# Optimization experiments

Hardware: AMD Instinct MI355X
Metric: run time of the kernel (lower is better)

Reference implementation:

```python
import jax, jax.numpy as jnp
import numpy as np

B, S, HID = 2, 2048, 2048
NH, NKV, HD = 16, 4, 128
ROT = 64            # head_dim * partial_rotary_factor
WINDOW = 512        # sliding_window_size
ROPE_BASE = 10000.0


def setup_inputs() -> dict:
    key = jax.random.key(0)
    ks = jax.random.split(key, 5)
    scale = 0.02
    return {
        "hidden_states": jax.random.normal(ks[0], (B, S, HID), jnp.float32),
        "Wq": jax.random.normal(ks[1], (NH * HD, HID), jnp.float32) * scale,
        "Wk": jax.random.normal(ks[2], (NKV * HD, HID), jnp.float32) * scale,
        "Wv": jax.random.normal(ks[3], (NKV * HD, HID), jnp.float32) * scale,
        "Wo": jax.random.normal(ks[4], (HID, NH * HD), jnp.float32) * scale,
    }


def _rope_cos_sin(seq_len, dtype):
    inv_freq = 1.0 / (ROPE_BASE ** (jnp.arange(0, ROT, 2, dtype=jnp.float32) / ROT))
    t = jnp.arange(seq_len, dtype=jnp.float32)
    freqs = t[:, None] * inv_freq[None, :]          # [S, ROT/2]
    emb = jnp.concatenate([freqs, freqs], axis=-1)   # [S, ROT]
    return jnp.cos(emb).astype(dtype), jnp.sin(emb).astype(dtype)


def _rotate_half(x):
    x1, x2 = x[..., : x.shape[-1] // 2], x[..., x.shape[-1] // 2:]
    return jnp.concatenate([-x2, x1], axis=-1)


def reference(hidden_states, Wq, Wk, Wv, Wo):
    b, s, _ = hidden_states.shape
    n_rep = NH // NKV

    q = (hidden_states @ Wq.T).reshape(b, s, NH, HD).transpose(0, 2, 1, 3)    # [B,NH,S,HD]
    k = (hidden_states @ Wk.T).reshape(b, s, NKV, HD).transpose(0, 2, 1, 3)   # [B,NKV,S,HD]
    v = (hidden_states @ Wv.T).reshape(b, s, NKV, HD).transpose(0, 2, 1, 3)

    # partial rotary embedding on the first ROT dims
    cos, sin = _rope_cos_sin(s, q.dtype)   # [S, ROT]
    cos = cos[None, None]                  # broadcast over batch, heads
    sin = sin[None, None]
    q_rot, q_pass = q[..., :ROT], q[..., ROT:]
    k_rot, k_pass = k[..., :ROT], k[..., ROT:]
    q_rot = q_rot * cos + _rotate_half(q_rot) * sin
    k_rot = k_rot * cos + _rotate_half(k_rot) * sin
    q = jnp.concatenate([q_rot, q_pass], axis=-1)
    k = jnp.concatenate([k_rot, k_pass], axis=-1)

    # GQA: repeat kv heads
    k = jnp.repeat(k, n_rep, axis=1)   # [B,NH,S,HD]
    v = jnp.repeat(v, n_rep, axis=1)

    scores = jnp.einsum("bhqd,bhkd->bhqk", q, k) / jnp.sqrt(jnp.asarray(HD, q.dtype))

    # sliding-window causal mask: allow j in [i-WINDOW+1, i]
    i = jnp.arange(s)[:, None]
    j = jnp.arange(s)[None, :]
    allowed = (j <= i) & (j > i - WINDOW)
    scores = jnp.where(allowed[None, None], scores, -jnp.inf)

    attn = jax.nn.softmax(scores.astype(jnp.float32), axis=-1).astype(q.dtype)
    out = jnp.einsum("bhqk,bhkd->bhqd", attn, v)          # [B,NH,S,HD]
    out = out.transpose(0, 2, 1, 3).reshape(b, s, NH * HD)
    return out @ Wo.T
```

## Files before the change

### kernel.cpp

```cpp
#include <hip/hip_runtime.h>
#include <cstdint>
#include <cstddef>

typedef __bf16 bf16;
typedef __attribute__((ext_vector_type(8))) __bf16 bf16x8;
typedef __attribute__((ext_vector_type(4))) __bf16 bf16x4;
typedef __attribute__((ext_vector_type(4))) float f32x4;
typedef __attribute__((ext_vector_type(4))) short s16x4;

#define S_LEN   2048
#define WIN     512
#define NH_Q    16
#define NH_KV   4
#define HD_     128
#define NTOK    4096

#if defined(__has_builtin)
#if __has_builtin(__builtin_amdgcn_mfma_f32_16x16x16bf16_1k)
#define HAVE_MFMA16 1
#endif
#endif
#ifndef HAVE_MFMA16
#define HAVE_MFMA16 0
#endif

#define WAIT_VM4   0x0F74
#define WAIT_VM3   0x0F73
#define WAIT_VM2   0x0F72
#define WAIT_VM0   0x0F70
#define CFENCE() __asm__ __volatile__("" ::: "memory")

__device__ __forceinline__ void async_copy16(const void* g, void* l) {
  __builtin_amdgcn_global_load_lds(
      (const __attribute__((address_space(1))) void*)g,
      (__attribute__((address_space(3))) void*)l, 16, 0, 0);
}

__global__ __launch_bounds__(256)
void cvt_all(const float* __restrict__ hs, const float* __restrict__ wq,
             const float* __restrict__ wk, const float* __restrict__ wv,
             const float* __restrict__ wo, bf16* __restrict__ hsb,
             bf16* __restrict__ wqb, bf16* __restrict__ wkb,
             bf16* __restrict__ wvb, bf16* __restrict__ wob) {
  long i = ((long)blockIdx.x * 256 + threadIdx.x) * 4;
  const float* in;
  bf16* out;
  if (i < 8388608)       { in = hs + i;            out = hsb + i; }
  else if (i < 12582912) { in = wq + (i - 8388608); out = wqb + (i - 8388608); }
  else if (i < 13631488) { in = wk + (i - 12582912); out = wkb + (i - 12582912); }
  else if (i < 14680064) { in = wv + (i - 13631488); out = wvb + (i - 13631488); }
  else                   { in = wo + (i - 14680064); out = wob + (i - 14680064); }
  float4 v = *(const float4*)in;
  bf16x4 t = {(bf16)v.x, (bf16)v.y, (bf16)v.z, (bf16)v.w};
  *(bf16x4*)out = t;
}

template <typename OutT>
__global__ __launch_bounds__(256)
void gemm_bt(const bf16* __restrict__ A, const bf16* __restrict__ W,
             OutT* __restrict__ C, int M, int N, int K) {
  __shared__ __align__(16) bf16 As[2][128 * 32];
  __shared__ __align__(16) bf16 Bs[2][128 * 32];
  const int tid  = threadIdx.x;
  const int wave = tid >> 6, lane = tid & 63;
  const int quad = lane >> 4, l16 = lane & 15;
  const int wm = wave >> 1, wn = wave & 1;
  const int m0 = blockIdx.y * 128, n0 = blockIdx.x * 128;
  const int lrow = lane >> 2;
  const int lcol = (((lane & 3) + ((lane >> 3) & 3)) & 3) * 8;
  const int gfrag = ((quad - ((l16 >> 1) & 3)) & 3) * 8;

  f32x4 acc[4][4];
#pragma unroll
  for (int i = 0; i < 4; ++i)
#pragma unroll
    for (int j = 0; j < 4; ++j) acc[i][j] = (f32x4){0.f, 0.f, 0.f, 0.f};

  auto stage = [&](int buf, int k0) {
#pragma unroll
    for (int it = 0; it < 2; ++it) {
      const int c   = it * 4 + wave;
      const int row = c * 16 + lrow;
      async_copy16(A + (size_t)(m0 + row) * K + k0 + lcol, &As[buf][c * 512]);
      async_copy16(W + (size_t)(n0 + row) * K + k0 + lcol, &Bs[buf][c * 512]);
    }
  };

  stage(0, 0);
  __syncthreads();
  for (int k0 = 0; k0 < K; k0 += 32) {
    const int cur = (k0 >> 5) & 1;
    if (k0 + 32 < K) stage(cur ^ 1, k0 + 32);
    bf16x8 af[4], bfr[4];
#pragma unroll
    for (int mt = 0; mt < 4; ++mt)
      af[mt] = *(const bf16x8*)&As[cur][(wm * 64 + mt * 16 + l16) * 32 + gfrag];
#pragma unroll
    for (int nt = 0; nt < 4; ++nt)
      bfr[nt] = *(const bf16x8*)&Bs[cur][(wn * 64 + nt * 16 + l16) * 32 + gfrag];
#pragma unroll
    for (int mt = 0; mt < 4; ++mt)
#pragma unroll
      for (int nt = 0; nt < 4; ++nt)
        acc[mt][nt] = __builtin_amdgcn_mfma_f32_16x16x32_bf16(
            af[mt], bfr[nt], acc[mt][nt], 0, 0, 0);
    __syncthreads();
  }
#pragma unroll
  for (int mt = 0; mt < 4; ++mt)
#pragma unroll
    for (int nt = 0; nt < 4; ++nt)
#pragma unroll
      for (int r = 0; r < 4; ++r) {
        const int row = m0 + wm * 64 + mt * 16 + quad * 4 + r;
        const int col = n0 + wn * 64 + nt * 16 + l16;
        C[(size_t)row * N + col] = (OutT)acc[mt][nt][r];
      }
}

__global__ __launch_bounds__(512, 2)
void gemm_qkv9(const bf16* __restrict__ A, const bf16* __restrict__ Wq,
               const bf16* __restrict__ Wk, const bf16* __restrict__ Wv,
               bf16* __restrict__ Qo, bf16* __restrict__ Ko,
               bf16* __restrict__ Vt) {
  __shared__ __align__(16) char smem[114688];
  const int tid  = threadIdx.x;
  const int wave = tid >> 6, lane = tid & 63;
  const int quad = lane >> 4, l16 = lane & 15;
  const int wm = wave >> 1, wn = wave & 1;

  const int flat = blockIdx.y * 16 + blockIdx.x;
  const int swz  = (flat & 7) * 32 + (flat >> 3);
  const int m0 = (swz >> 4) * 256;
  const int n0 = (swz & 15) * 192;

  const int rdb = (l16 * 64 + quad * 16) ^ ((l16 & 8) << 2);

  const int srow = lane >> 2;
  const int scol = ((lane & 3) * 8) ^ ((lane >> 5) << 4);

  const int rbA0 = (wave >> 1) * 4 + (wave & 1);
  const int rbA1 = rbA0 + 2;
  const bf16* a0p = A + (size_t)(m0 + rbA0 * 16 + srow) * 2048 + scol;
  const bf16* a1p = A + (size_t)(m0 + rbA1 * 16 + srow) * 2048 + scol;
  const int da0 = (rbA0 * 2) << 10;
  const int da1 = (rbA1 * 2) << 10;

  const int rbB0 = wave >> 1, khB0 = wave & 1;
  const int rbB1 = 4 + wave;
  const int nrow0 = n0 + rbB0 * 16 + srow;
  const int nrow1 = n0 + rbB1 * 16 + srow;
  const bf16* b0p = (nrow0 < 2048 ? Wq + (size_t)nrow0 * 2048
                   : nrow0 < 2560 ? Wk + (size_t)(nrow0 - 2048) * 2048
                                  : Wv + (size_t)(nrow0 - 2560) * 2048)
                    + scol + khB0 * 32;
  const bf16* b1p = (nrow1 < 2048 ? Wq + (size_t)nrow1 * 2048
                   : nrow1 < 2560 ? Wk + (size_t)(nrow1 - 2048) * 2048
                                  : Wv + (size_t)(nrow1 - 2560) * 2048)
                    + scol;
  const int db0 = (rbB0 * 2 + khB0) << 10;
  const int db1 = (rbB1 * 2) << 10;

#define STAGE_A0(tt) do { char* _b = smem + ((tt) & 1) * 32768;        \
    async_copy16(a0p + (tt) * 64,      _b + da0);                      \
    async_copy16(a0p + (tt) * 64 + 32, _b + da0 + 1024); } while (0)
#define STAGE_A1(tt) do { char* _b = smem + ((tt) & 1) * 32768;        \
    async_copy16(a1p + (tt) * 64,      _b + da1);                      \
    async_copy16(a1p + (tt) * 64 + 32, _b + da1 + 1024); } while (0)
#define STAGE_B0(tt) do { char* _b = smem + 65536 + ((tt) & 1) * 24576; \
    async_copy16(b0p + (tt) * 64,      _b + db0); } while (0)
#define STAGE_B12(tt) do { char* _b = smem + 65536 + ((tt) & 1) * 24576; \
    async_copy16(b1p + (tt) * 64,      _b + db1);                      \
    async_copy16(b1p + (tt) * 64 + 32, _b + db1 + 1024); } while (0)

  f32x4 acc[4][6];
#pragma unroll
  for (int i = 0; i < 4; ++i)
#pragma unroll
    for (int j = 0; j < 6; ++j) acc[i][j] = (f32x4){0.f, 0.f, 0.f, 0.f};

  bf16x8 afr[2][2];
  bf16x8 bfr[6][2];

  auto read_a = [&](const char* Ab, int mh) __attribute__((always_inline)) {
#pragma unroll
    for (int mt2 = 0; mt2 < 2; ++mt2)
#pragma unroll
      for (int ks = 0; ks < 2; ++ks)
        afr[mt2][ks] = *(const bf16x8*)(
            Ab + (((wm * 4 + mh * 2 + mt2) * 2 + ks) << 10) + rdb);
  };
  auto read_b = [&](const char* Bb, int jlo, int jhi) __attribute__((always_inline)) {
#pragma unroll
    for (int j = 0; j < 6; ++j) {
      if (j < jlo || j > jhi) continue;
      const int cc = (j >> 1) * 4 + (j & 1) * 2 + wn;
#pragma unroll
      for (int ks = 0; ks < 2; ++ks)
        bfr[j][ks] = *(const bf16x8*)(Bb + ((cc * 2 + ks) << 10) + rdb);
    }
  };
  auto do_mfma = [&](int mh, int jlo, int jhi) __attribute__((always_inline)) {
    __builtin_amdgcn_s_setprio(1);
#pragma unroll
    for (int mt2 = 0; mt2 < 2; ++mt2)
#pragma unroll
      for (int j = 0; j < 6; ++j) {
        if (j < jlo || j > jhi) continue;
#pragma unroll
        for (int ks = 0; ks < 2; ++ks)
          acc[mh * 2 + mt2][j] = __builtin_amdgcn_mfma_f32_16x16x32_bf16(
              afr[mt2][ks], bfr[j][ks], acc[mh * 2 + mt2][j], 0, 0, 0);
      }
    __builtin_amdgcn_s_setprio(0);
  };

  STAGE_A0(0); STAGE_B0(0); STAGE_B12(0); STAGE_A1(0);
  CFENCE();

  for (int t = 0; t < 31; ++t) {
    const char* Ab = smem + (t & 1) * 32768;
    const char* Bb = smem + 65536 + (t & 1) * 24576;
    const int nx = t + 1;
    __builtin_amdgcn_s_waitcnt(WAIT_VM4); CFENCE();
    __builtin_amdgcn_s_barrier(); CFENCE();
    read_a(Ab, 0); read_b(Bb, 0, 1);
    STAGE_A0(nx); CFENCE();
    do_mfma(0, 0, 1);
    __builtin_amdgcn_s_waitcnt(WAIT_VM4); CFENCE();
    __builtin_amdgcn_s_barrier(); CFENCE();
    read_b(Bb, 2, 5);
    STAGE_B0(nx); CFENCE();
    do_mfma(0, 2, 5);
    __builtin_amdgcn_s_waitcnt(WAIT_VM3); CFENCE();
    __builtin_amdgcn_s_barrier(); CFENCE();
    read_a(Ab, 1);
    STAGE_B12(nx); CFENCE();
    do_mfma(1, 0, 1);
    __builtin_amdgcn_s_barrier(); CFENCE();
    STAGE_A1(nx); CFENCE();
    do_mfma(1, 2, 5);
  }
  {
    const char* Ab = smem + 32768;
    const char* Bb = smem + 65536 + 24576;
    __builtin_amdgcn_s_waitcnt(WAIT_VM4); CFENCE();
    __builtin_amdgcn_s_barrier(); CFENCE();
    read_a(Ab, 0); read_b(Bb, 0, 1);
    do_mfma(0, 0, 1);
    __builtin_amdgcn_s_waitcnt(WAIT_VM2); CFENCE();
    __builtin_amdgcn_s_barrier(); CFENCE();
    read_b(Bb, 2, 5);
    do_mfma(0, 2, 5);
    __builtin_amdgcn_s_waitcnt(WAIT_VM0); CFENCE();
    __builtin_amdgcn_s_barrier(); CFENCE();
    read_a(Ab, 1);
    do_mfma(1, 0, 1);
    do_mfma(1, 2, 5);
  }
#undef STAGE_A0
#undef STAGE_A1
#undef STAGE_B0
#undef STAGE_B12

  {
    const float d = (float)(wn * 16 + l16);
    const float invf = exp2f(-d * 0.41524101186091903f);
#pragma unroll
    for (int b = 0; b < 3; ++b) {
      const int cb = n0 + b * 64;
      if (cb < 2560 && (cb & 127) == 0) {
#pragma unroll
        for (int mt = 0; mt < 4; ++mt)
#pragma unroll
          for (int r = 0; r < 4; ++r) {
            const int pos = (m0 + wm * 64 + mt * 16 + quad * 4 + r) & (S_LEN - 1);
            float s, c;
            __sincosf((float)pos * invf, &s, &c);
            const float x1 = acc[mt][2 * b][r], x2 = acc[mt][2 * b + 1][r];
            acc[mt][2 * b][r]     = x1 * c - x2 * s;
            acc[mt][2 * b + 1][r] = x2 * c + x1 * s;
          }
      }
    }
  }
#pragma unroll
  for (int mt = 0; mt < 4; ++mt) {
    const int row0 = m0 + wm * 64 + mt * 16 + quad * 4;
#pragma unroll
    for (int j = 0; j < 6; ++j) {
      const int col16 = n0 + (j >> 1) * 64 + ((j & 1) * 2 + wn) * 16;
      if (col16 < 2048) {
#pragma unroll
        for (int r = 0; r < 4; ++r)
          Qo[(size_t)(row0 + r) * 2048 + col16 + l16] = (bf16)acc[mt][j][r];
      } else if (col16 < 2560) {
#pragma unroll
        for (int r = 0; r < 4; ++r)
          Ko[(size_t)(row0 + r) * 512 + col16 - 2048 + l16] = (bf16)acc[mt][j][r];
      } else {
        const int colv = col16 + l16 - 2560;
        const int bb = row0 >> 11, s0 = row0 & (S_LEN - 1);
        bf16x4 tq = {(bf16)acc[mt][j][0], (bf16)acc[mt][j][1],
                     (bf16)acc[mt][j][2], (bf16)acc[mt][j][3]};
        *(bf16x4*)(Vt + ((size_t)(bb * NH_KV + (colv >> 7)) * HD_ + (colv & 127))
                        * S_LEN + s0) = tq;
      }
    }
  }
}

#define KS_STRIDE 136
#define VT_STRIDE 72

__global__ __launch_bounds__(256)
void attn_kernel(const bf16* __restrict__ Qg, const bf16* __restrict__ Kg,
                 const bf16* __restrict__ Vtg, bf16* __restrict__ Og) {
  __shared__ __align__(16) bf16 Ks[64 * KS_STRIDE];
  __shared__ __align__(16) bf16 Vt[128 * VT_STRIDE];
#if !HAVE_MFMA16
  __shared__ __align__(16) bf16 Pb[4][16 * 72];
#endif
  const int tid  = threadIdx.x;
  const int wave = tid >> 6, lane = tid & 63;
  const int quad = lane >> 4, l16 = lane & 15;
  const int qt = blockIdx.x, h = blockIdx.y, b = blockIdx.z;
  const int kv = h >> 2;
  const int q0 = qt * 64;
  const int tok0 = b * S_LEN;
  const float scale = 0.08838834764831845f;
  const int q = q0 + wave * 16 + l16;

  bf16x8 qf[4];
  {
    const bf16* qp = Qg + (size_t)(tok0 + q) * (NH_Q * HD_) + h * HD_ + quad * 8;
#pragma unroll
    for (int kb = 0; kb < 4; ++kb) qf[kb] = *(const bf16x8*)(qp + kb * 32);
  }

  f32x4 o[8];
#pragma unroll
  for (int dt = 0; dt < 8; ++dt) o[dt] = (f32x4){0.f, 0.f, 0.f, 0.f};
  float m_run = -__builtin_inff(), l_run = 0.f;

  int kt_begin = q0 - WIN;
  if (kt_begin < 0) kt_begin = 0;
  const int kt_end = q0 + 64;
  const bf16* vt_base = Vtg + (size_t)(b * NH_KV + kv) * HD_ * S_LEN;

  for (int kt = kt_begin; kt < kt_end; kt += 64) {
    __syncthreads();
#pragma unroll
    for (int it = 0; it < 4; ++it) {
      int vid = tid + it * 256;
      int key = vid >> 4, dblk = vid & 15;
      bf16x8 v = *(const bf16x8*)(Kg + (size_t)(tok0 + kt + key) * (NH_KV * HD_)
                                  + kv * HD_ + dblk * 8);
      *(bf16x8*)&Ks[key * KS_STRIDE + dblk * 8] = v;
    }
#pragma unroll
    for (int it = 0; it < 4; ++it) {
      int vid = tid + it * 256;
      int d = vid >> 3, kblk = vid & 7;
      bf16x8 v = *(const bf16x8*)(vt_base + (size_t)d * S_LEN + kt + kblk * 8);
      *(bf16x8*)&Vt[d * VT_STRIDE + kblk * 8] = v;
    }
    __syncthreads();

    f32x4 st[4];
#pragma unroll
    for (int nt = 0; nt < 4; ++nt) {
      f32x4 acc = (f32x4){0.f, 0.f, 0.f, 0.f};
#pragma unroll
      for (int kb = 0; kb < 4; ++kb) {
        bf16x8 kf = *(const bf16x8*)&Ks[(nt * 16 + l16) * KS_STRIDE + kb * 32 + quad * 8];
        acc = __builtin_amdgcn_mfma_f32_16x16x32_bf16(kf, qf[kb], acc, 0, 0, 0);
      }
      st[nt] = acc;
    }
#pragma unroll
    for (int nt = 0; nt < 4; ++nt)
#pragma unroll
      for (int r = 0; r < 4; ++r) {
        int key = kt + nt * 16 + quad * 4 + r;
        bool ok = (key <= q) && (key > q - WIN);
        st[nt][r] = ok ? st[nt][r] * scale : -__builtin_inff();
      }
    float mx = -__builtin_inff();
#pragma unroll
    for (int nt = 0; nt < 4; ++nt)
#pragma unroll
      for (int r = 0; r < 4; ++r) mx = fmaxf(mx, st[nt][r]);
    mx = fmaxf(mx, __shfl_xor(mx, 16, 64));
    mx = fmaxf(mx, __shfl_xor(mx, 32, 64));
    float mnew = fmaxf(m_run, mx);
    float msub = (mnew == -__builtin_inff()) ? 0.f : mnew;
    float alpha = __expf(m_run - msub);
    m_run = mnew;
    float p[4][4], psum = 0.f;
#pragma unroll
    for (int nt = 0; nt < 4; ++nt)
#pragma unroll
      for (int r = 0; r < 4; ++r) {
        p[nt][r] = __expf(st[nt][r] - msub);
        psum += p[nt][r];
      }
    psum += __shfl_xor(psum, 16, 64);
    psum += __shfl_xor(psum, 32, 64);
    l_run = l_run * alpha + psum;
#pragma unroll
    for (int dt = 0; dt < 8; ++dt) o[dt] *= alpha;

#if HAVE_MFMA16
    s16x4 pb[4];
#pragma unroll
    for (int nt = 0; nt < 4; ++nt)
#pragma unroll
      for (int r = 0; r < 4; ++r) {
        union { __bf16 h; short s; } u;
        u.h = (bf16)p[nt][r];
        pb[nt][r] = u.s;
      }
#pragma unroll
    for (int dt = 0; dt < 8; ++dt)
#pragma unroll
      for (int nt = 0; nt < 4; ++nt) {
        s16x4 vf = *(const s16x4*)&Vt[(dt * 16 + l16) * VT_STRIDE + nt * 16 + quad * 4];
        o[dt] = __builtin_amdgcn_mfma_f32_16x16x16bf16_1k(vf, pb[nt], o[dt], 0, 0, 0);
      }
#else
#pragma unroll
    for (int nt = 0; nt < 4; ++nt) {
      bf16x4 t;
#pragma unroll
      for (int r = 0; r < 4; ++r) t[r] = (bf16)p[nt][r];
      *(bf16x4*)&Pb[wave][l16 * 72 + nt * 16 + quad * 4] = t;
    }
    __syncthreads();
    bf16x8 pf[2];
    pf[0] = *(const bf16x8*)&Pb[wave][l16 * 72 + quad * 8];
    pf[1] = *(const bf16x8*)&Pb[wave][l16 * 72 + 32 + quad * 8];
#pragma unroll
    for (int dt = 0; dt < 8; ++dt)
#pragma unroll
      for (int kb = 0; kb < 2; ++kb) {
        bf16x8 vf = *(const bf16x8*)&Vt[(dt * 16 + l16) * VT_STRIDE + kb * 32 + quad * 8];
        o[dt] = __builtin_amdgcn_mfma_f32_16x16x32_bf16(vf, pf[kb], o[dt], 0, 0, 0);
      }
#endif
  }

  float inv = 1.f / l_run;
  __syncthreads();
#pragma unroll
  for (int dt = 0; dt < 8; ++dt) {
    bf16x4 t;
#pragma unroll
    for (int r = 0; r < 4; ++r) t[r] = (bf16)(o[dt][r] * inv);
    *(bf16x4*)&Ks[(wave * 16 + l16) * KS_STRIDE + dt * 16 + quad * 4] = t;
  }
  __syncthreads();
#pragma unroll
  for (int it = 0; it < 4; ++it) {
    int idx = tid + it * 256;
    int row = idx >> 4, chunk = idx & 15;
    bf16x8 v = *(const bf16x8*)&Ks[row * KS_STRIDE + chunk * 8];
    *(bf16x8*)(Og + (size_t)(tok0 + q0 + row) * (NH_Q * HD_) + h * HD_ + chunk * 8) = v;
  }
}

extern "C" void kernel_launch(void* const* d_in, const int* in_sizes, int n_in,
                              void* d_out, int out_size, void* d_ws, size_t ws_size,
                              hipStream_t stream) {
  const float* hs = (const float*)d_in[0];
  const float* Wq = (const float*)d_in[1];
  const float* Wk = (const float*)d_in[2];
  const float* Wv = (const float*)d_in[3];
  const float* Wo = (const float*)d_in[4];
  float* out = (float*)d_out;

  char* w = (char*)d_ws;
  bf16* hsb = (bf16*)w; w += (size_t)NTOK * 2048 * 2;
  bf16* wqb = (bf16*)w; w += (size_t)2048 * 2048 * 2;
  bf16* wkb = (bf16*)w; w += (size_t)512 * 2048 * 2;
  bf16* wvb = (bf16*)w; w += (size_t)512 * 2048 * 2;
  bf16* wob = (bf16*)w; w += (size_t)2048 * 2048 * 2;
  bf16* qb  = (bf16*)w; w += (size_t)NTOK * 2048 * 2;
  bf16* kb  = (bf16*)w; w += (size_t)NTOK * 512 * 2;
  bf16* vtb = (bf16*)w; w += (size_t)NTOK * 512 * 2;
  bf16* ab  = hsb;

  cvt_all<<<18874368 / 1024, 256, 0, stream>>>(hs, Wq, Wk, Wv, Wo,
                                               hsb, wqb, wkb, wvb, wob);

  gemm_qkv9<<<dim3(16, 16), 512, 0, stream>>>(hsb, wqb, wkb, wvb,
                                              qb, kb, vtb);

  attn_kernel<<<dim3(S_LEN / 64, NH_Q, 2), 256, 0, stream>>>(qb, kb, vtb, ab);

  gemm_bt<float><<<dim3(2048 / 128, NTOK / 128), 256, 0, stream>>>(
      ab, wob, out, NTOK, 2048, 2048);
}
```

Before: 256.4 us.

## Replace output projection GEMM with 8-wave 256x128 pipelined kernel

Swaps the generic 128x128 tile, 4-wave output-projection GEMM for a specialized 512-thread kernel. The new kernel uses 256x128 tiles with K-step 64, XOR-swizzled LDS, and block-index swizzling for L2 locality. It splits each K step into four phases that interleave async global-to-LDS staging with MFMA work under explicit waitcnt/barrier control and s_setprio. This is meant to hide load latency and raise MFMA utilization, at the cost of hardcoded shapes and fragile manual synchronization.

```diff
diff --git a/kernel.cpp b/kernel.cpp
--- a/kernel.cpp
+++ b/kernel.cpp
@@ -55,20 +55,50 @@
   *(bf16x4*)out = t;
 }
 
-template <typename OutT>
-__global__ __launch_bounds__(256)
-void gemm_bt(const bf16* __restrict__ A, const bf16* __restrict__ W,
-             OutT* __restrict__ C, int M, int N, int K) {
-  __shared__ __align__(16) bf16 As[2][128 * 32];
-  __shared__ __align__(16) bf16 Bs[2][128 * 32];
+__global__ __launch_bounds__(512, 2)
+void gemm_out8(const bf16* __restrict__ A, const bf16* __restrict__ W,
+               float* __restrict__ C) {
+  __shared__ __align__(16) char smem[98304];
   const int tid  = threadIdx.x;
   const int wave = tid >> 6, lane = tid & 63;
   const int quad = lane >> 4, l16 = lane & 15;
   const int wm = wave >> 1, wn = wave & 1;
-  const int m0 = blockIdx.y * 128, n0 = blockIdx.x * 128;
-  const int lrow = lane >> 2;
-  const int lcol = (((lane & 3) + ((lane >> 3) & 3)) & 3) * 8;
-  const int gfrag = ((quad - ((l16 >> 1) & 3)) & 3) * 8;
+
+  const int flat = blockIdx.y * 16 + blockIdx.x;
+  const int swz  = (flat & 7) * 32 + (flat >> 3);
+  const int m0 = (swz >> 4) * 256;
+  const int n0 = (swz & 15) * 128;
+
+  const int rdb = (l16 * 64 + quad * 16) ^ ((l16 & 8) << 2);
+  const int srow = lane >> 2;
+  const int scol = ((lane & 3) * 8) ^ ((lane >> 5) << 4);
+
+  const bf16* aptr[2][2];
+  int adst[2][2];
+#pragma unroll
+  for (int mh = 0; mh < 2; ++mh)
+#pragma unroll
+    for (int j = 0; j < 2; ++j) {
+      const int rb = (wave >> 1) * 4 + mh * 2 + j;
+      aptr[mh][j] = A + (size_t)(m0 + rb * 16 + srow) * 2048 + scol
+                    + (wave & 1) * 32;
+      adst[mh][j] = (rb * 2 + (wave & 1)) << 10;
+    }
+  const bf16* bptr[2];
+  int bdst[2];
+#pragma unroll
+  for (int nh = 0; nh < 2; ++nh) {
+    const int cb = (wave >> 2) * 4 + nh * 2 + ((wave >> 1) & 1);
+    bptr[nh] = W + (size_t)(n0 + cb * 16 + srow) * 2048 + scol
+               + (wave & 1) * 32;
+    bdst[nh] = (cb * 2 + (wave & 1)) << 10;
+  }
+
+#define STAGE_A(mh, tt) do { char* _b = smem + ((tt) & 1) * 32768;      \
+    async_copy16(aptr[mh][0] + (tt) * 64, _b + adst[mh][0]);            \
+    async_copy16(aptr[mh][1] + (tt) * 64, _b + adst[mh][1]); } while (0)
+#define STAGE_B(nh, tt) do { char* _b = smem + 65536 + ((tt) & 1) * 16384; \
+    async_copy16(bptr[nh] + (tt) * 64, _b + bdst[nh]); } while (0)
 
   f32x4 acc[4][4];
 #pragma unroll
@@ -76,36 +106,85 @@
 #pragma unroll
     for (int j = 0; j < 4; ++j) acc[i][j] = (f32x4){0.f, 0.f, 0.f, 0.f};
 
-  auto stage = [&](int buf, int k0) {
-#pragma unroll
-    for (int it = 0; it < 2; ++it) {
-      const int c   = it * 4 + wave;
-      const int row = c * 16 + lrow;
-      async_copy16(A + (size_t)(m0 + row) * K + k0 + lcol, &As[buf][c * 512]);
-      async_copy16(W + (size_t)(n0 + row) * K + k0 + lcol, &Bs[buf][c * 512]);
-    }
+  bf16x8 afr[2][2];
+  bf16x8 bfr[2][2][2];
+
+  auto read_a = [&](const char* Ab, int mh) __attribute__((always_inline)) {
+#pragma unroll
+    for (int mt2 = 0; mt2 < 2; ++mt2)
+#pragma unroll
+      for (int ks = 0; ks < 2; ++ks)
+        afr[mt2][ks] = *(const bf16x8*)(
+            Ab + (((wm * 4 + mh * 2 + mt2) * 2 + ks) << 10) + rdb);
   };
-
-  stage(0, 0);
-  __syncthreads();
-  for (int k0 = 0; k0 < K; k0 += 32) {
-    const int cur = (k0 >> 5) & 1;
-    if (k0 + 32 < K) stage(cur ^ 1, k0 + 32);
-    bf16x8 af[4], bfr[4];
-#pragma unroll
-    for (int mt = 0; mt < 4; ++mt)
-      af[mt] = *(const bf16x8*)&As[cur][(wm * 64 + mt * 16 + l16) * 32 + gfrag];
-#pragma unroll
-    for (int nt = 0; nt < 4; ++nt)
-      bfr[nt] = *(const bf16x8*)&Bs[cur][(wn * 64 + nt * 16 + l16) * 32 + gfrag];
-#pragma unroll
-    for (int mt = 0; mt < 4; ++mt)
-#pragma unroll
-      for (int nt = 0; nt < 4; ++nt)
-        acc[mt][nt] = __builtin_amdgcn_mfma_f32_16x16x32_bf16(
-            af[mt], bfr[nt], acc[mt][nt], 0, 0, 0);
-    __syncthreads();
-  }
+  auto read_b = [&](const char* Bb, int nh) __attribute__((always_inline)) {
+#pragma unroll
+    for (int nt2 = 0; nt2 < 2; ++nt2)
+#pragma unroll
+      for (int ks = 0; ks < 2; ++ks)
+        bfr[nh][nt2][ks] = *(const bf16x8*)(
+            Bb + (((wn * 4 + nh * 2 + nt2) * 2 + ks) << 10) + rdb);
+  };
+  auto do_mfma = [&](int mh, int nh) __attribute__((always_inline)) {
+    __builtin_amdgcn_s_setprio(1);
+#pragma unroll
+    for (int mt2 = 0; mt2 < 2; ++mt2)
+#pragma unroll
+      for (int nt2 = 0; nt2 < 2; ++nt2)
+#pragma unroll
+        for (int ks = 0; ks < 2; ++ks)
+          acc[mh * 2 + mt2][nh * 2 + nt2] = __builtin_amdgcn_mfma_f32_16x16x32_bf16(
+              afr[mt2][ks], bfr[nh][nt2][ks], acc[mh * 2 + mt2][nh * 2 + nt2],
+              0, 0, 0);
+    __builtin_amdgcn_s_setprio(0);
+  };
+
+  STAGE_A(0, 0); STAGE_B(0, 0); STAGE_B(1, 0); STAGE_A(1, 0);
+  CFENCE();
+
+  for (int t = 0; t < 31; ++t) {
+    const char* Ab = smem + (t & 1) * 32768;
+    const char* Bb = smem + 65536 + (t & 1) * 16384;
+    const int nx = t + 1;
+    __builtin_amdgcn_s_waitcnt(WAIT_VM3); CFENCE();
+    __builtin_amdgcn_s_barrier(); CFENCE();
+    read_a(Ab, 0); read_b(Bb, 0);
+    STAGE_A(0, nx); CFENCE();
+    do_mfma(0, 0);
+    __builtin_amdgcn_s_waitcnt(WAIT_VM4); CFENCE();
+    __builtin_amdgcn_s_barrier(); CFENCE();
+    read_b(Bb, 1);
+    STAGE_B(0, nx); CFENCE();
+    do_mfma(0, 1);
+    __builtin_amdgcn_s_waitcnt(WAIT_VM3); CFENCE();
+    __builtin_amdgcn_s_barrier(); CFENCE();
+    read_a(Ab, 1);
+    STAGE_B(1, nx); CFENCE();
+    do_mfma(1, 0);
+    __builtin_amdgcn_s_barrier(); CFENCE();
+    STAGE_A(1, nx); CFENCE();
+    do_mfma(1, 1);
+  }
+  {
+    const char* Ab = smem + 32768;
+    const char* Bb = smem + 65536 + 16384;
+    __builtin_amdgcn_s_waitcnt(WAIT_VM3); CFENCE();
+    __builtin_amdgcn_s_barrier(); CFENCE();
+    read_a(Ab, 0); read_b(Bb, 0);
+    do_mfma(0, 0);
+    __builtin_amdgcn_s_waitcnt(WAIT_VM2); CFENCE();
+    __builtin_amdgcn_s_barrier(); CFENCE();
+    read_b(Bb, 1);
+    do_mfma(0, 1);
+    __builtin_amdgcn_s_waitcnt(WAIT_VM0); CFENCE();
+    __builtin_amdgcn_s_barrier(); CFENCE();
+    read_a(Ab, 1);
+    do_mfma(1, 0);
+    do_mfma(1, 1);
+  }
+#undef STAGE_A
+#undef STAGE_B
+
 #pragma unroll
   for (int mt = 0; mt < 4; ++mt)
 #pragma unroll
@@ -114,7 +193,7 @@
       for (int r = 0; r < 4; ++r) {
         const int row = m0 + wm * 64 + mt * 16 + quad * 4 + r;
         const int col = n0 + wn * 64 + nt * 16 + l16;
-        C[(size_t)row * N + col] = (OutT)acc[mt][nt][r];
+        C[(size_t)row * 2048 + col] = acc[mt][nt][r];
       }
 }
 
@@ -498,6 +577,5 @@
 
   attn_kernel<<<dim3(S_LEN / 64, NH_Q, 2), 256, 0, stream>>>(qb, kb, vtb, ab);
 
-  gemm_bt<float><<<dim3(2048 / 128, NTOK / 128), 256, 0, stream>>>(
-      ab, wob, out, NTOK, 2048, 2048);
+  gemm_out8<<<dim3(16, 16), 512, 0, stream>>>(ab, wob, out);
 }
```

After: 244.2 us. 4.8% less time.
